# Kernel optimization log

Measured on AMD Instinct MI355X. Metric: run time of the kernel, lower is better.

## Reference

```python
import jax, jax.numpy as jnp
from jax import lax
import numpy as np

B, T, I, H = 4096, 200, 32, 6  # batch, seq_len, input_size, hidden


def _lstm_layer(x_seq, W_ih, W_hh, b_ih, b_hh):
    """Single unidirectional LSTM layer, PyTorch gate order (i,f,g,o).
    x_seq: [B,T,Din]. Returns (all_h [B,T,H], h_last [B,H])."""
    Bb = x_seq.shape[0]
    Hh = W_hh.shape[1]
    # Precompute input projections for all timesteps (hoisted out of the scan).
    x_proj = jnp.einsum('bti,gi->btg', x_seq, W_ih) + b_ih + b_hh  # [B,T,4H]

    def step(carry, xp_t):
        h, c = carry
        gates = xp_t + h @ W_hh.T  # [B,4H]
        i_g, f_g, g_g, o_g = jnp.split(gates, 4, axis=-1)
        i_g = jax.nn.sigmoid(i_g)
        f_g = jax.nn.sigmoid(f_g)
        g_g = jnp.tanh(g_g)
        o_g = jax.nn.sigmoid(o_g)
        c = f_g * c + i_g * g_g
        h = o_g * jnp.tanh(c)
        return (h, c), h

    init = (jnp.zeros((Bb, Hh), x_seq.dtype), jnp.zeros((Bb, Hh), x_seq.dtype))
    (h_last, _), hs = lax.scan(step, init, jnp.swapaxes(x_proj, 0, 1))  # time-major scan
    return jnp.swapaxes(hs, 0, 1), h_last


def setup_inputs() -> dict:
    key = jax.random.key(0)
    ks = jax.random.split(key, 11)
    s = 0.2  # ~ uniform(-1/sqrt(H)) scale for H=6
    inp = {
        'x': jax.random.normal(ks[0], (B, T, I), dtype=jnp.float32),
        'W_ih0': jax.random.normal(ks[1], (4 * H, I), dtype=jnp.float32) * s,
        'W_hh0': jax.random.normal(ks[2], (4 * H, H), dtype=jnp.float32) * s,
        'b_ih0': jax.random.normal(ks[3], (4 * H,), dtype=jnp.float32) * s,
        'b_hh0': jax.random.normal(ks[4], (4 * H,), dtype=jnp.float32) * s,
        'W_ih1': jax.random.normal(ks[5], (4 * H, H), dtype=jnp.float32) * s,
        'W_hh1': jax.random.normal(ks[6], (4 * H, H), dtype=jnp.float32) * s,
        'b_ih1': jax.random.normal(ks[7], (4 * H,), dtype=jnp.float32) * s,
        'b_hh1': jax.random.normal(ks[8], (4 * H,), dtype=jnp.float32) * s,
        'W_lin': jax.random.normal(ks[9], (1, H), dtype=jnp.float32) * s,
        'b_lin': jax.random.normal(ks[10], (1,), dtype=jnp.float32) * s,
    }
    return inp


def reference(x, W_ih0, W_hh0, b_ih0, b_hh0, W_ih1, W_hh1, b_ih1, b_hh1, W_lin, b_lin):
    # Layer 0 (eval mode: inter-layer dropout disabled)
    h1_seq, _ = _lstm_layer(x, W_ih0, W_hh0, b_ih0, b_hh0)
    # Layer 1
    _, h2_last = _lstm_layer(h1_seq, W_ih1, W_hh1, b_ih1, b_hh1)
    # Linear head on last layer's final hidden state: [B,1]
    return h2_last @ W_lin.T + b_lin
```

## Files before the change

kernel.cpp:

```cpp
#include <hip/hip_runtime.h>


#define TLEN  200
#define ISZ   32
#define HSZ   6
#define RPITCH 25
#define WPITCH 36
#define RING_DW (64 * RPITCH)
#define WOFF  RING_DW
#define BOFF  (WOFF + 24 * WPITCH)
#define LDS_DW (BOFF + 24)

__device__ __forceinline__ float fast_sig(float x) {
    return __builtin_amdgcn_rcpf(1.0f + __expf(-x));
}
__device__ __forceinline__ float rl(float v, int l) {
    return __int_as_float(__builtin_amdgcn_readlane(__float_as_int(v), l));
}
template <int CTRL>
__device__ __forceinline__ float qperm(float v) {
    return __int_as_float(__builtin_amdgcn_mov_dpp(__float_as_int(v), CTRL, 0xf, 0xf, true));
}
__device__ __forceinline__ float dot4(float4 w, float4 v) {
    return fmaf(w.x, v.x, fmaf(w.y, v.y, fmaf(w.z, v.z, w.w * v.w)));
}

__global__ __launch_bounds__(64) void lstm_one(
    const float* __restrict__ x,
    const float* __restrict__ Wih0, const float* __restrict__ Whh0,
    const float* __restrict__ bih0, const float* __restrict__ bhh0,
    const float* __restrict__ Wih1, const float* __restrict__ Whh1,
    const float* __restrict__ bih1, const float* __restrict__ bhh1,
    const float* __restrict__ Wlin, const float* __restrict__ blin,
    float* __restrict__ out)
{
    __shared__ float lds[LDS_DW];

    const int lane = threadIdx.x;
    const int b    = blockIdx.x;

    const int o = lane & 1;
    const int L = lane >> 1;

    const bool loHalf = (lane < 32);
    const int  p  = lane & 3;
    const int  jq = (lane & 31) >> 2;
    const int  j  = (jq < HSZ) ? jq : 0;
    const int  r  = 6 * p + j;

#define LDSW(ROW, KCQ) (*(const float4*)&lds[WOFF + (o * 12 + (ROW)) * WPITCH + ((KCQ) << 2)])

#pragma unroll
    for (int k = 0; k < 13; ++k) {
        const int idx = lane + (k << 6);
        if (idx < 768) {
            const int row = idx >> 5, kk = idx & 31;
            lds[WOFF + row * WPITCH + kk] = Wih0[idx];
        } else if (idx < 792) {
            lds[BOFF + idx - 768] = bih0[idx - 768] + bhh0[idx - 768];
        }
    }

    float WA[6], WB[6], base1 = 0.0f, sgc = 1.0f, tgc = 0.0f;
#pragma unroll
    for (int k = 0; k < 6; ++k) { WA[k] = 0.0f; WB[k] = 0.0f; }
    if (loHalf) {
#pragma unroll
        for (int k = 0; k < 6; ++k) WA[k] = Whh0[r * 6 + k];
    } else {
#pragma unroll
        for (int k = 0; k < 6; ++k) { WA[k] = Wih1[r * 6 + k]; WB[k] = Whh1[r * 6 + k]; }
        base1 = bih1[r] + bhh1[r];
    }
    if (p == 2) {
#pragma unroll
        for (int k = 0; k < 6; ++k) { WA[k] *= 2.0f; WB[k] *= 2.0f; }
        base1 *= 2.0f; sgc = 2.0f; tgc = -1.0f;
    }

    const float* xb = x + (size_t)b * TLEN * ISZ;

#pragma unroll
    for (int w01 = 0; w01 < 2; ++w01) {
        const int t = (w01 << 5) + L;
        const float4* xr4 = (const float4*)(xb + t * ISZ);
        float4 xw[8];
#pragma unroll
        for (int q = 0; q < 8; ++q) xw[q] = xr4[q];
        float a0c[12];
#pragma unroll
        for (int jj = 0; jj < 12; ++jj) a0c[jj] = 0.0f;
#pragma unroll
        for (int kc = 0; kc < 8; ++kc)
#pragma unroll
            for (int jj = 0; jj < 12; ++jj)
                a0c[jj] += dot4(LDSW(jj, kc), xw[kc]);
#pragma unroll
        for (int jj = 0; jj < 12; ++jj) {
            float v = a0c[jj] + lds[BOFF + o * 12 + jj];
            if (jj < 6) v = (o == 1) ? v * 2.0f : v;
            lds[t * RPITCH + o * 12 + jj] = v;
        }
    }

    float acc[12];
#pragma unroll
    for (int jj = 0; jj < 12; ++jj) acc[jj] = 0.0f;
    const float* pc = xb + (size_t)min(64 + L, TLEN - 1) * ISZ;
    const float* pn = xb + (size_t)min(96 + L, TLEN - 1) * ISZ;
    float4 f0, f1;
    f1 = *((const float4*)pc);
    float4 Wp0 = LDSW(0, 0), Wp1 = LDSW(1, 0), Wp2 = LDSW(2, 0);

    float c = 0.0f, h = 0.0f;
    float xp_cur = lds[r];

#define KC_HEAD(KC) do { \
    f0 = f1; \
    const float4* _srcp = ((KC) < 7) ? ((const float4*)pc + (KC) + 1) \
                                     : ((const float4*)pn); \
    f1 = *_srcp; \
} while (0)

#define SPREAD_STEP(RT, KC) do { \
    acc[3*(RT)+0] += dot4(Wp0, f0); \
    acc[3*(RT)+1] += dot4(Wp1, f0); \
    acc[3*(RT)+2] += dot4(Wp2, f0); \
    const int _rtn = ((RT) + 1) & 3; \
    const int _kcn = ((RT) == 3) ? (((KC) + 1) & 7) : (KC); \
    Wp0 = LDSW(3*_rtn + 0, _kcn); \
    Wp1 = LDSW(3*_rtn + 1, _kcn); \
    Wp2 = LDSW(3*_rtn + 2, _kcn); \
} while (0)

#define SCAN_STEP(ITV) do { \
    const float h10=rl(h,0),  h11=rl(h,4),  h12=rl(h,8); \
    const float h13=rl(h,12), h14=rl(h,16), h15=rl(h,20); \
    const float h20=rl(h,32), h21=rl(h,36), h22=rl(h,40); \
    const float h23=rl(h,44), h24=rl(h,48), h25=rl(h,52); \
    const float _xn = lds[(((ITV) + 1) & 63) * RPITCH + r]; \
    const float _g0 = loHalf ? xp_cur : base1; \
    const float _a0 = fmaf(WA[0],h10, fmaf(WA[2],h12, fmaf(WA[4],h14, _g0))); \
    const float _a1 = fmaf(WA[1],h11, fmaf(WA[3],h13, WA[5]*h15)); \
    const float _b0 = fmaf(WB[0],h20, fmaf(WB[2],h22, WB[4]*h24)); \
    const float _b1 = fmaf(WB[1],h21, fmaf(WB[3],h23, WB[5]*h25)); \
    const float _g  = (_a0 + _a1) + (_b0 + _b1); \
    const float _aG = fmaf(sgc, fast_sig(_g), tgc); \
    const float _iq = qperm<0x00>(_aG), _fq = qperm<0x55>(_aG); \
    const float _gq = qperm<0xAA>(_aG), _oq = qperm<0xFF>(_aG); \
    c = fmaf(_fq, c, _iq * _gq); \
    const float _th = fmaf(2.0f, fast_sig(2.0f * c), -1.0f); \
    h = _oq * _th; \
    xp_cur = _xn; \
    if ((ITV) == 200) { \
        float _s = blin[0]; \
        _s = fmaf(Wlin[0], rl(h, 32), _s); \
        _s = fmaf(Wlin[1], rl(h, 36), _s); \
        _s = fmaf(Wlin[2], rl(h, 40), _s); \
        _s = fmaf(Wlin[3], rl(h, 44), _s); \
        _s = fmaf(Wlin[4], rl(h, 48), _s); \
        _s = fmaf(Wlin[5], rl(h, 52), _s); \
        if (lane == 0) out[b] = _s; \
    } \
} while (0)

#define ENTRY(IT0) do { \
    const int _slot = ((IT0) + 32 + L) & 63; \
    _Pragma("unroll") \
    for (int _jj = 0; _jj < 12; ++_jj) { \
        float _v = acc[_jj] + lds[BOFF + o * 12 + _jj]; \
        if (_jj < 6) _v = (o == 1) ? _v * 2.0f : _v; \
        lds[_slot * RPITCH + o * 12 + _jj] = _v; \
        acc[_jj] = 0.0f; \
    } \
    pc = pn; \
    pn = xb + (size_t)min((IT0) + 96 + L, TLEN - 1) * ISZ; \
} while (0)

    KC_HEAD(0);
    SPREAD_STEP(0, 0);
    {
        const float g  = loHalf ? xp_cur : base1;
        const float aG = fmaf(sgc, fast_sig(g), tgc);
        const float iq = qperm<0x00>(aG), gq = qperm<0xAA>(aG), oq = qperm<0xFF>(aG);
        const float cn = iq * gq;
        const float th = fmaf(2.0f, fast_sig(2.0f * cn), -1.0f);
        c = loHalf ? cn : 0.0f;
        h = loHalf ? (oq * th) : 0.0f;
        xp_cur = lds[RPITCH + r];
    }

    SPREAD_STEP(1, 0); SCAN_STEP(1);
    SPREAD_STEP(2, 0); SCAN_STEP(2);
    SPREAD_STEP(3, 0); SCAN_STEP(3);
    for (int kc = 1; kc < 8; ++kc) {
        KC_HEAD(kc);
        const int itb = kc << 2;
        SPREAD_STEP(0, kc); SCAN_STEP(itb + 0);
        SPREAD_STEP(1, kc); SCAN_STEP(itb + 1);
        SPREAD_STEP(2, kc); SCAN_STEP(itb + 2);
        SPREAD_STEP(3, kc); SCAN_STEP(itb + 3);
    }

    for (int w = 1; w < 7; ++w) {
        const int it0 = w << 5;
        ENTRY(it0);
        for (int kc = 0; kc < 8; ++kc) {
            const int itb = it0 + (kc << 2);
            if (itb > 200) break;
            KC_HEAD(kc);
            SPREAD_STEP(0, kc); SCAN_STEP(itb + 0);
            SPREAD_STEP(1, kc); SCAN_STEP(itb + 1);
            SPREAD_STEP(2, kc); SCAN_STEP(itb + 2);
            SPREAD_STEP(3, kc); SCAN_STEP(itb + 3);
        }
    }

#undef LDSW
#undef KC_HEAD
#undef SPREAD_STEP
#undef SCAN_STEP
#undef ENTRY
}

extern "C" void kernel_launch(void* const* d_in, const int* in_sizes, int n_in,
                              void* d_out, int out_size, void* d_ws, size_t ws_size,
                              hipStream_t stream) {
    const float* x    = (const float*)d_in[0];
    const float* Wih0 = (const float*)d_in[1];
    const float* Whh0 = (const float*)d_in[2];
    const float* bih0 = (const float*)d_in[3];
    const float* bhh0 = (const float*)d_in[4];
    const float* Wih1 = (const float*)d_in[5];
    const float* Whh1 = (const float*)d_in[6];
    const float* bih1 = (const float*)d_in[7];
    const float* bhh1 = (const float*)d_in[8];
    const float* Wlin = (const float*)d_in[9];
    const float* blin = (const float*)d_in[10];
    float* out = (float*)d_out;

    lstm_one<<<4096, 64, 0, stream>>>(x, Wih0, Whh0, bih0, bhh0,
                                      Wih1, Whh1, bih1, bhh1,
                                      Wlin, blin, out);
}
```

Before: 249.8 us.

## Split input projection into a producer wave feeding the scan wave via LDS

Adds a second wavefront per block that computes the layer-0 input projections for 32-timestep windows into a double-buffered LDS ring. The original wave now runs only the recurrent scan, with raised scheduling priority, and the two waves sync with barriers at each window boundary. This takes the projection FMAs and global x loads off the serial scan's critical path. In exchange it doubles threads per block, which may reduce resident blocks, and adds barrier stalls each window.

```diff
diff --git a/kernel.cpp b/kernel.cpp
--- a/kernel.cpp
+++ b/kernel.cpp
@@ -25,7 +25,7 @@
     return fmaf(w.x, v.x, fmaf(w.y, v.y, fmaf(w.z, v.z, w.w * v.w)));
 }
 
-__global__ __launch_bounds__(64) void lstm_one(
+__global__ __launch_bounds__(128) void lstm_one(
     const float* __restrict__ x,
     const float* __restrict__ Wih0, const float* __restrict__ Whh0,
     const float* __restrict__ bih0, const float* __restrict__ bhh0,
@@ -36,11 +36,68 @@
 {
     __shared__ float lds[LDS_DW];
 
-    const int lane = threadIdx.x;
+    const int tid  = threadIdx.x;
+    const int lane = tid & 63;
     const int b    = blockIdx.x;
-
-    const int o = lane & 1;
-    const int L = lane >> 1;
+    const float* xb = x + (size_t)b * TLEN * ISZ;
+
+    if (tid >= 64) {
+        const int o = lane & 1;
+        const int L = lane >> 1;
+#define LDSW(ROW, KCQ) (*(const float4*)&lds[WOFF + (o * 12 + (ROW)) * WPITCH + ((KCQ) << 2)])
+
+#pragma unroll
+        for (int k = 0; k < 13; ++k) {
+            const int idx = lane + (k << 6);
+            if (idx < 768) {
+                const int row = idx >> 5, kk = idx & 31;
+                lds[WOFF + row * WPITCH + kk] = Wih0[idx];
+            } else if (idx < 792) {
+                lds[BOFF + idx - 768] = bih0[idx - 768] + bhh0[idx - 768];
+            }
+        }
+
+        float a0c[12];
+        auto PROJW = [&](int w) {
+            const int t = (w << 5) + L;
+            const float4* xr4 = (const float4*)(xb + (size_t)min(t, TLEN - 1) * ISZ);
+#pragma unroll
+            for (int jj = 0; jj < 12; ++jj) a0c[jj] = 0.0f;
+#pragma unroll
+            for (int hh = 0; hh < 2; ++hh) {
+                float4 xw[4];
+#pragma unroll
+                for (int q = 0; q < 4; ++q) xw[q] = xr4[(hh << 2) + q];
+#pragma unroll
+                for (int kc = 0; kc < 4; ++kc)
+#pragma unroll
+                    for (int jj = 0; jj < 12; ++jj)
+                        a0c[jj] += dot4(LDSW(jj, (hh << 2) + kc), xw[kc]);
+            }
+        };
+        auto WRITEW = [&](int w) {
+            const int slot = ((w << 5) + L) & 63;
+#pragma unroll
+            for (int jj = 0; jj < 12; ++jj) {
+                float v = a0c[jj] + lds[BOFF + o * 12 + jj];
+                if (jj < 6) v = (o == 1) ? v * 2.0f : v;
+                lds[slot * RPITCH + o * 12 + jj] = v;
+            }
+        };
+
+        PROJW(0); WRITEW(0);
+        PROJW(1); WRITEW(1);
+        __syncthreads();
+#pragma unroll 1
+        for (int w = 2; w < 7; ++w) {
+            PROJW(w);
+            __syncthreads();
+            WRITEW(w);
+            __syncthreads();
+        }
+#undef LDSW
+        return;
+    }
 
     const bool loHalf = (lane < 32);
     const int  p  = lane & 3;
@@ -48,19 +105,6 @@
     const int  j  = (jq < HSZ) ? jq : 0;
     const int  r  = 6 * p + j;
 
-#define LDSW(ROW, KCQ) (*(const float4*)&lds[WOFF + (o * 12 + (ROW)) * WPITCH + ((KCQ) << 2)])
-
-#pragma unroll
-    for (int k = 0; k < 13; ++k) {
-        const int idx = lane + (k << 6);
-        if (idx < 768) {
-            const int row = idx >> 5, kk = idx & 31;
-            lds[WOFF + row * WPITCH + kk] = Wih0[idx];
-        } else if (idx < 792) {
-            lds[BOFF + idx - 768] = bih0[idx - 768] + bhh0[idx - 768];
-        }
-    }
-
     float WA[6], WB[6], base1 = 0.0f, sgc = 1.0f, tgc = 0.0f;
 #pragma unroll
     for (int k = 0; k < 6; ++k) { WA[k] = 0.0f; WB[k] = 0.0f; }
@@ -78,72 +122,24 @@
         base1 *= 2.0f; sgc = 2.0f; tgc = -1.0f;
     }
 
-    const float* xb = x + (size_t)b * TLEN * ISZ;
-
-#pragma unroll
-    for (int w01 = 0; w01 < 2; ++w01) {
-        const int t = (w01 << 5) + L;
-        const float4* xr4 = (const float4*)(xb + t * ISZ);
-        float4 xw[8];
-#pragma unroll
-        for (int q = 0; q < 8; ++q) xw[q] = xr4[q];
-        float a0c[12];
-#pragma unroll
-        for (int jj = 0; jj < 12; ++jj) a0c[jj] = 0.0f;
-#pragma unroll
-        for (int kc = 0; kc < 8; ++kc)
-#pragma unroll
-            for (int jj = 0; jj < 12; ++jj)
-                a0c[jj] += dot4(LDSW(jj, kc), xw[kc]);
-#pragma unroll
-        for (int jj = 0; jj < 12; ++jj) {
-            float v = a0c[jj] + lds[BOFF + o * 12 + jj];
-            if (jj < 6) v = (o == 1) ? v * 2.0f : v;
-            lds[t * RPITCH + o * 12 + jj] = v;
-        }
-    }
-
-    float acc[12];
-#pragma unroll
-    for (int jj = 0; jj < 12; ++jj) acc[jj] = 0.0f;
-    const float* pc = xb + (size_t)min(64 + L, TLEN - 1) * ISZ;
-    const float* pn = xb + (size_t)min(96 + L, TLEN - 1) * ISZ;
-    float4 f0, f1;
-    f1 = *((const float4*)pc);
-    float4 Wp0 = LDSW(0, 0), Wp1 = LDSW(1, 0), Wp2 = LDSW(2, 0);
-
+    __syncthreads();
+    __builtin_amdgcn_s_setprio(1);
+
+    int xoff = r;
     float c = 0.0f, h = 0.0f;
-    float xp_cur = lds[r];
-
-#define KC_HEAD(KC) do { \
-    f0 = f1; \
-    const float4* _srcp = ((KC) < 7) ? ((const float4*)pc + (KC) + 1) \
-                                     : ((const float4*)pn); \
-    f1 = *_srcp; \
-} while (0)
-
-#define SPREAD_STEP(RT, KC) do { \
-    acc[3*(RT)+0] += dot4(Wp0, f0); \
-    acc[3*(RT)+1] += dot4(Wp1, f0); \
-    acc[3*(RT)+2] += dot4(Wp2, f0); \
-    const int _rtn = ((RT) + 1) & 3; \
-    const int _kcn = ((RT) == 3) ? (((KC) + 1) & 7) : (KC); \
-    Wp0 = LDSW(3*_rtn + 0, _kcn); \
-    Wp1 = LDSW(3*_rtn + 1, _kcn); \
-    Wp2 = LDSW(3*_rtn + 2, _kcn); \
-} while (0)
-
-#define SCAN_STEP(ITV) do { \
-    const float h10=rl(h,0),  h11=rl(h,4),  h12=rl(h,8); \
-    const float h13=rl(h,12), h14=rl(h,16), h15=rl(h,20); \
-    const float h20=rl(h,32), h21=rl(h,36), h22=rl(h,40); \
-    const float h23=rl(h,44), h24=rl(h,48), h25=rl(h,52); \
-    const float _xn = lds[(((ITV) + 1) & 63) * RPITCH + r]; \
+    float xp_cur = lds[xoff];
+
+#define SCAN_STEP(XN) do { \
+    const float h10 = rl(h, 0),  h11 = rl(h, 4),  h12 = rl(h, 8); \
+    const float h13 = rl(h, 12), h14 = rl(h, 16), h15 = rl(h, 20); \
+    const float h20 = rl(h, 32), h21 = rl(h, 36), h22 = rl(h, 40); \
+    const float h23 = rl(h, 44), h24 = rl(h, 48), h25 = rl(h, 52); \
+    const float _xn = (XN); \
     const float _g0 = loHalf ? xp_cur : base1; \
-    const float _a0 = fmaf(WA[0],h10, fmaf(WA[2],h12, fmaf(WA[4],h14, _g0))); \
-    const float _a1 = fmaf(WA[1],h11, fmaf(WA[3],h13, WA[5]*h15)); \
-    const float _b0 = fmaf(WB[0],h20, fmaf(WB[2],h22, WB[4]*h24)); \
-    const float _b1 = fmaf(WB[1],h21, fmaf(WB[3],h23, WB[5]*h25)); \
+    const float _a0 = fmaf(WA[0], h10, fmaf(WA[2], h12, fmaf(WA[4], h14, _g0))); \
+    const float _a1 = fmaf(WA[1], h11, fmaf(WA[3], h13, WA[5] * h15)); \
+    const float _b0 = fmaf(WB[0], h20, fmaf(WB[2], h22, WB[4] * h24)); \
+    const float _b1 = fmaf(WB[1], h21, fmaf(WB[3], h23, WB[5] * h25)); \
     const float _g  = (_a0 + _a1) + (_b0 + _b1); \
     const float _aG = fmaf(sgc, fast_sig(_g), tgc); \
     const float _iq = qperm<0x00>(_aG), _fq = qperm<0x55>(_aG); \
@@ -152,33 +148,8 @@
     const float _th = fmaf(2.0f, fast_sig(2.0f * c), -1.0f); \
     h = _oq * _th; \
     xp_cur = _xn; \
-    if ((ITV) == 200) { \
-        float _s = blin[0]; \
-        _s = fmaf(Wlin[0], rl(h, 32), _s); \
-        _s = fmaf(Wlin[1], rl(h, 36), _s); \
-        _s = fmaf(Wlin[2], rl(h, 40), _s); \
-        _s = fmaf(Wlin[3], rl(h, 44), _s); \
-        _s = fmaf(Wlin[4], rl(h, 48), _s); \
-        _s = fmaf(Wlin[5], rl(h, 52), _s); \
-        if (lane == 0) out[b] = _s; \
-    } \
 } while (0)
 
-#define ENTRY(IT0) do { \
-    const int _slot = ((IT0) + 32 + L) & 63; \
-    _Pragma("unroll") \
-    for (int _jj = 0; _jj < 12; ++_jj) { \
-        float _v = acc[_jj] + lds[BOFF + o * 12 + _jj]; \
-        if (_jj < 6) _v = (o == 1) ? _v * 2.0f : _v; \
-        lds[_slot * RPITCH + o * 12 + _jj] = _v; \
-        acc[_jj] = 0.0f; \
-    } \
-    pc = pn; \
-    pn = xb + (size_t)min((IT0) + 96 + L, TLEN - 1) * ISZ; \
-} while (0)
-
-    KC_HEAD(0);
-    SPREAD_STEP(0, 0);
     {
         const float g  = loHalf ? xp_cur : base1;
         const float aG = fmaf(sgc, fast_sig(g), tgc);
@@ -187,40 +158,33 @@
         const float th = fmaf(2.0f, fast_sig(2.0f * cn), -1.0f);
         c = loHalf ? cn : 0.0f;
         h = loHalf ? (oq * th) : 0.0f;
-        xp_cur = lds[RPITCH + r];
-    }
-
-    SPREAD_STEP(1, 0); SCAN_STEP(1);
-    SPREAD_STEP(2, 0); SCAN_STEP(2);
-    SPREAD_STEP(3, 0); SCAN_STEP(3);
-    for (int kc = 1; kc < 8; ++kc) {
-        KC_HEAD(kc);
-        const int itb = kc << 2;
-        SPREAD_STEP(0, kc); SCAN_STEP(itb + 0);
-        SPREAD_STEP(1, kc); SCAN_STEP(itb + 1);
-        SPREAD_STEP(2, kc); SCAN_STEP(itb + 2);
-        SPREAD_STEP(3, kc); SCAN_STEP(itb + 3);
-    }
-
-    for (int w = 1; w < 7; ++w) {
-        const int it0 = w << 5;
-        ENTRY(it0);
-        for (int kc = 0; kc < 8; ++kc) {
-            const int itb = it0 + (kc << 2);
-            if (itb > 200) break;
-            KC_HEAD(kc);
-            SPREAD_STEP(0, kc); SCAN_STEP(itb + 0);
-            SPREAD_STEP(1, kc); SCAN_STEP(itb + 1);
-            SPREAD_STEP(2, kc); SCAN_STEP(itb + 2);
-            SPREAD_STEP(3, kc); SCAN_STEP(itb + 3);
-        }
-    }
-
-#undef LDSW
-#undef KC_HEAD
-#undef SPREAD_STEP
+        xp_cur = lds[xoff + RPITCH];
+    }
+
+#pragma unroll 1
+    for (int w = 0; w < 6; ++w) {
+        if (w > 0) SCAN_STEP(lds[xoff + RPITCH]);
+#pragma unroll
+        for (int k = 1; k <= 30; ++k) SCAN_STEP(lds[xoff + (k + 1) * RPITCH]);
+        xoff ^= 800;
+        SCAN_STEP(lds[xoff]);
+        if (w < 5) { __syncthreads(); __syncthreads(); }
+    }
+
+#pragma unroll
+    for (int k = 0; k < 8; ++k) SCAN_STEP(lds[xoff + (k + 1) * RPITCH]);
+    SCAN_STEP(lds[xoff + 9 * RPITCH]);
+    {
+        float s = blin[0];
+        s = fmaf(Wlin[0], rl(h, 32), s);
+        s = fmaf(Wlin[1], rl(h, 36), s);
+        s = fmaf(Wlin[2], rl(h, 40), s);
+        s = fmaf(Wlin[3], rl(h, 44), s);
+        s = fmaf(Wlin[4], rl(h, 48), s);
+        s = fmaf(Wlin[5], rl(h, 52), s);
+        if (lane == 0) out[b] = s;
+    }
 #undef SCAN_STEP
-#undef ENTRY
 }
 
 extern "C" void kernel_launch(void* const* d_in, const int* in_sizes, int n_in,
@@ -239,7 +203,7 @@
     const float* blin = (const float*)d_in[10];
     float* out = (float*)d_out;
 
-    lstm_one<<<4096, 64, 0, stream>>>(x, Wih0, Whh0, bih0, bhh0,
-                                      Wih1, Whh1, bih1, bhh1,
-                                      Wlin, blin, out);
-}
+    lstm_one<<<4096, 128, 0, stream>>>(x, Wih0, Whh0, bih0, bhh0,
+                                       Wih1, Whh1, bih1, bhh1,
+                                       Wlin, blin, out);
+}
```

After: 355.0 us. +42.1%, slower.

## Split LSTM into global-memory input projection phase then recurrent scan

Applied to the files above, without the earlier changes.

Adds a kernel variant that first computes all layer-0 input projections for a sequence and writes them to a workspace buffer in global memory. It then runs the two-layer recurrence as a separate phase that prefetches projections from that buffer, four steps ahead. This replaces the interleaved LDS ring that mixed projection math into the scan, shrinking LDS use and simplifying the critical recurrent loop. The cost is about 78 MB of extra global write and read traffic, plus a full wait before the scan starts. The old fused kernel remains as a fallback when the workspace is too small.

```diff
diff --git a/kernel.cpp b/kernel.cpp
--- a/kernel.cpp
+++ b/kernel.cpp
@@ -4,12 +4,17 @@
 #define TLEN  200
 #define ISZ   32
 #define HSZ   6
+#define WPITCH 36
+
+#define PWOFF 0
+#define PBOFF (24 * WPITCH)
+#define PLDS_DW (PBOFF + 24)
+
 #define RPITCH 25
-#define WPITCH 36
 #define RING_DW (64 * RPITCH)
-#define WOFF  RING_DW
-#define BOFF  (WOFF + 24 * WPITCH)
-#define LDS_DW (BOFF + 24)
+#define FWOFF  RING_DW
+#define FBOFF  (FWOFF + 24 * WPITCH)
+#define FLDS_DW (FBOFF + 24)
 
 __device__ __forceinline__ float fast_sig(float x) {
     return __builtin_amdgcn_rcpf(1.0f + __expf(-x));
@@ -25,7 +30,170 @@
     return fmaf(w.x, v.x, fmaf(w.y, v.y, fmaf(w.z, v.z, w.w * v.w)));
 }
 
-__global__ __launch_bounds__(64) void lstm_one(
+__global__ __launch_bounds__(64) void lstm_split(
+    const float* __restrict__ x,
+    const float* __restrict__ Wih0, const float* __restrict__ Whh0,
+    const float* __restrict__ bih0, const float* __restrict__ bhh0,
+    const float* __restrict__ Wih1, const float* __restrict__ Whh1,
+    const float* __restrict__ bih1, const float* __restrict__ bhh1,
+    const float* __restrict__ Wlin, const float* __restrict__ blin,
+    float* __restrict__ out, float* __restrict__ xp)
+{
+    __shared__ float lds[PLDS_DW];
+
+    const int lane = threadIdx.x;
+    const int b    = blockIdx.x;
+    const float* xb  = x  + (size_t)b * TLEN * ISZ;
+    float*       xpb = xp + (size_t)b * TLEN * 24;
+
+    {
+        const int o = lane & 1;
+        const int L = lane >> 1;
+#define LDSW(ROW, KCQ) (*(const float4*)&lds[PWOFF + (o * 12 + (ROW)) * WPITCH + ((KCQ) << 2)])
+
+#pragma unroll
+        for (int k = 0; k < 13; ++k) {
+            const int idx = lane + (k << 6);
+            if (idx < 768) {
+                const int row = idx >> 5, kk = idx & 31;
+                lds[PWOFF + row * WPITCH + kk] = Wih0[idx];
+            } else if (idx < 792) {
+                lds[PBOFF + idx - 768] = bih0[idx - 768] + bhh0[idx - 768];
+            }
+        }
+
+#pragma unroll 1
+        for (int k7 = 0; k7 < 7; ++k7) {
+            const int t = (k7 << 5) + L;
+            if (t < TLEN) {
+                const float4* xr4 = (const float4*)(xb + (size_t)t * ISZ);
+                float a0c[12];
+#pragma unroll
+                for (int jj = 0; jj < 12; ++jj) a0c[jj] = 0.0f;
+#pragma unroll
+                for (int hh = 0; hh < 2; ++hh) {
+                    float4 xw[4];
+#pragma unroll
+                    for (int q = 0; q < 4; ++q) xw[q] = xr4[(hh << 2) + q];
+#pragma unroll
+                    for (int jh = 0; jh < 2; ++jh)
+#pragma unroll
+                        for (int kc = 0; kc < 4; ++kc)
+#pragma unroll
+                            for (int jj = jh * 6; jj < jh * 6 + 6; ++jj)
+                                a0c[jj] += dot4(LDSW(jj, (hh << 2) + kc), xw[kc]);
+                }
+                float vv[12];
+#pragma unroll
+                for (int jj = 0; jj < 12; ++jj) {
+                    float v = a0c[jj] + lds[PBOFF + o * 12 + jj];
+                    if (jj < 6) v = (o == 1) ? v * 2.0f : v;
+                    vv[jj] = v;
+                }
+                float4* dst = (float4*)(xpb + t * 24 + o * 12);
+                dst[0] = make_float4(vv[0], vv[1], vv[2],  vv[3]);
+                dst[1] = make_float4(vv[4], vv[5], vv[6],  vv[7]);
+                dst[2] = make_float4(vv[8], vv[9], vv[10], vv[11]);
+            }
+        }
+#undef LDSW
+    }
+
+    asm volatile("s_waitcnt vmcnt(0)" ::: "memory");
+
+    const bool loHalf = (lane < 32);
+    const int  p  = lane & 3;
+    const int  jq = (lane & 31) >> 2;
+    const int  j  = (jq < HSZ) ? jq : 0;
+    const int  r  = 6 * p + j;
+
+    float WA[6], WB[6], base1 = 0.0f, sgc = 1.0f, tgc = 0.0f;
+#pragma unroll
+    for (int k = 0; k < 6; ++k) { WA[k] = 0.0f; WB[k] = 0.0f; }
+    if (loHalf) {
+#pragma unroll
+        for (int k = 0; k < 6; ++k) WA[k] = Whh0[r * 6 + k];
+    } else {
+#pragma unroll
+        for (int k = 0; k < 6; ++k) { WA[k] = Wih1[r * 6 + k]; WB[k] = Whh1[r * 6 + k]; }
+        base1 = bih1[r] + bhh1[r];
+    }
+    if (p == 2) {
+#pragma unroll
+        for (int k = 0; k < 6; ++k) { WA[k] *= 2.0f; WB[k] *= 2.0f; }
+        base1 *= 2.0f; sgc = 2.0f; tgc = -1.0f;
+    }
+
+    const float* xr = xpb + r;
+    float xp0 = xr[0];
+    float q0 = xr[24], q1 = xr[48], q2 = xr[72], q3 = xr[96];
+
+    float c = 0.0f, h = 0.0f;
+
+#define SSTEP(XPV) do { \
+    const float h10 = rl(h, 0),  h11 = rl(h, 4),  h12 = rl(h, 8); \
+    const float h13 = rl(h, 12), h14 = rl(h, 16), h15 = rl(h, 20); \
+    const float h20 = rl(h, 32), h21 = rl(h, 36), h22 = rl(h, 40); \
+    const float h23 = rl(h, 44), h24 = rl(h, 48), h25 = rl(h, 52); \
+    const float _g0 = loHalf ? (XPV) : base1; \
+    const float _a0 = fmaf(WA[0], h10, fmaf(WA[2], h12, fmaf(WA[4], h14, _g0))); \
+    const float _a1 = fmaf(WA[1], h11, fmaf(WA[3], h13, WA[5] * h15)); \
+    const float _b0 = fmaf(WB[0], h20, fmaf(WB[2], h22, WB[4] * h24)); \
+    const float _b1 = fmaf(WB[1], h21, fmaf(WB[3], h23, WB[5] * h25)); \
+    const float _g  = (_a0 + _a1) + (_b0 + _b1); \
+    const float _aG = fmaf(sgc, fast_sig(_g), tgc); \
+    const float _iq = qperm<0x00>(_aG), _fq = qperm<0x55>(_aG); \
+    const float _gq = qperm<0xAA>(_aG), _oq = qperm<0xFF>(_aG); \
+    c = fmaf(_fq, c, _iq * _gq); \
+    const float _th = fmaf(2.0f, fast_sig(2.0f * c), -1.0f); \
+    h = _oq * _th; \
+} while (0)
+
+    {
+        const float g  = loHalf ? xp0 : base1;
+        const float aG = fmaf(sgc, fast_sig(g), tgc);
+        const float iq = qperm<0x00>(aG), gq = qperm<0xAA>(aG), oq = qperm<0xFF>(aG);
+        const float cn = iq * gq;
+        const float th = fmaf(2.0f, fast_sig(2.0f * cn), -1.0f);
+        c = loHalf ? cn : 0.0f;
+        h = loHalf ? (oq * th) : 0.0f;
+    }
+
+    const float* P = xr + 24;
+#pragma unroll 1
+    for (int bod = 0; bod < 24; ++bod) {
+        SSTEP(q0); q0 = P[4 * 24];
+        SSTEP(q1); q1 = P[5 * 24];
+        SSTEP(q2); q2 = P[6 * 24];
+        SSTEP(q3); q3 = P[7 * 24];
+        SSTEP(q0); q0 = P[8 * 24];
+        SSTEP(q1); q1 = P[9 * 24];
+        SSTEP(q2); q2 = P[10 * 24];
+        SSTEP(q3); q3 = P[11 * 24];
+        P += 8 * 24;
+    }
+    SSTEP(q0); q0 = P[4 * 24];
+    SSTEP(q1); q1 = P[5 * 24];
+    SSTEP(q2); q2 = P[6 * 24];
+    SSTEP(q3);
+    SSTEP(q0);
+    SSTEP(q1);
+    SSTEP(q2);
+    SSTEP(q3);
+    {
+        float s = blin[0];
+        s = fmaf(Wlin[0], rl(h, 32), s);
+        s = fmaf(Wlin[1], rl(h, 36), s);
+        s = fmaf(Wlin[2], rl(h, 40), s);
+        s = fmaf(Wlin[3], rl(h, 44), s);
+        s = fmaf(Wlin[4], rl(h, 48), s);
+        s = fmaf(Wlin[5], rl(h, 52), s);
+        if (lane == 0) out[b] = s;
+    }
+#undef SSTEP
+}
+
+__global__ __launch_bounds__(64) void lstm_fb(
     const float* __restrict__ x,
     const float* __restrict__ Wih0, const float* __restrict__ Whh0,
     const float* __restrict__ bih0, const float* __restrict__ bhh0,
@@ -34,7 +202,7 @@
     const float* __restrict__ Wlin, const float* __restrict__ blin,
     float* __restrict__ out)
 {
-    __shared__ float lds[LDS_DW];
+    __shared__ float lds[FLDS_DW];
 
     const int lane = threadIdx.x;
     const int b    = blockIdx.x;
@@ -48,16 +216,16 @@
     const int  j  = (jq < HSZ) ? jq : 0;
     const int  r  = 6 * p + j;
 
-#define LDSW(ROW, KCQ) (*(const float4*)&lds[WOFF + (o * 12 + (ROW)) * WPITCH + ((KCQ) << 2)])
+#define LDSW(ROW, KCQ) (*(const float4*)&lds[FWOFF + (o * 12 + (ROW)) * WPITCH + ((KCQ) << 2)])
 
 #pragma unroll
     for (int k = 0; k < 13; ++k) {
         const int idx = lane + (k << 6);
         if (idx < 768) {
             const int row = idx >> 5, kk = idx & 31;
-            lds[WOFF + row * WPITCH + kk] = Wih0[idx];
+            lds[FWOFF + row * WPITCH + kk] = Wih0[idx];
         } else if (idx < 792) {
-            lds[BOFF + idx - 768] = bih0[idx - 768] + bhh0[idx - 768];
+            lds[FBOFF + idx - 768] = bih0[idx - 768] + bhh0[idx - 768];
         }
     }
 
@@ -97,7 +265,7 @@
                 a0c[jj] += dot4(LDSW(jj, kc), xw[kc]);
 #pragma unroll
         for (int jj = 0; jj < 12; ++jj) {
-            float v = a0c[jj] + lds[BOFF + o * 12 + jj];
+            float v = a0c[jj] + lds[FBOFF + o * 12 + jj];
             if (jj < 6) v = (o == 1) ? v * 2.0f : v;
             lds[t * RPITCH + o * 12 + jj] = v;
         }
@@ -168,7 +336,7 @@
     const int _slot = ((IT0) + 32 + L) & 63; \
     _Pragma("unroll") \
     for (int _jj = 0; _jj < 12; ++_jj) { \
-        float _v = acc[_jj] + lds[BOFF + o * 12 + _jj]; \
+        float _v = acc[_jj] + lds[FBOFF + o * 12 + _jj]; \
         if (_jj < 6) _v = (o == 1) ? _v * 2.0f : _v; \
         lds[_slot * RPITCH + o * 12 + _jj] = _v; \
         acc[_jj] = 0.0f; \
@@ -239,7 +407,14 @@
     const float* blin = (const float*)d_in[10];
     float* out = (float*)d_out;
 
-    lstm_one<<<4096, 64, 0, stream>>>(x, Wih0, Whh0, bih0, bhh0,
-                                      Wih1, Whh1, bih1, bhh1,
-                                      Wlin, blin, out);
-}
+    const size_t XP_BYTES = (size_t)4096 * TLEN * 24 * sizeof(float);
+    if (d_ws != nullptr && ws_size >= XP_BYTES) {
+        lstm_split<<<4096, 64, 0, stream>>>(x, Wih0, Whh0, bih0, bhh0,
+                                            Wih1, Whh1, bih1, bhh1,
+                                            Wlin, blin, out, (float*)d_ws);
+    } else {
+        lstm_fb<<<4096, 64, 0, stream>>>(x, Wih0, Whh0, bih0, bhh0,
+                                         Wih1, Whh1, bih1, bhh1,
+                                         Wlin, blin, out);
+    }
+}
```

New measurement: 268.6 us. +7.5%, slower.

## Split LSTM into projection kernel and packed 4-batch-per-wave scan kernel

Applied to the files above, without the earlier changes.

Replaces the single fused kernel with two kernels when a workspace is available. The first computes the layer-0 input projections for all timesteps into global memory. The second runs the recurrence with four batch elements per 64-lane wave, each lane owning one hidden unit and computing all four gates, with ds_swizzle broadcasts instead of readlane. This packs lanes more densely and removes the in-loop projection work from the serial chain. In exchange it writes and reads about 79 MB of projections through global memory. It keeps the old kernel as a fallback.

```diff
diff --git a/kernel.cpp b/kernel.cpp
--- a/kernel.cpp
+++ b/kernel.cpp
@@ -4,15 +4,26 @@
 #define TLEN  200
 #define ISZ   32
 #define HSZ   6
+#define WPITCH 36
+
+#define PWOFF 0
+#define PBOFF (24 * WPITCH)
+#define PLDS_DW (PBOFF + 24)
+
 #define RPITCH 25
-#define WPITCH 36
 #define RING_DW (64 * RPITCH)
-#define WOFF  RING_DW
-#define BOFF  (WOFF + 24 * WPITCH)
-#define LDS_DW (BOFF + 24)
+#define FWOFF  RING_DW
+#define FBOFF  (FWOFF + 24 * WPITCH)
+#define FLDS_DW (FBOFF + 24)
+
+#define XP4_COUNT ((size_t)4096 * TLEN * 6)
+#define WS_REQ    ((XP4_COUNT + 6) * 16)
 
 __device__ __forceinline__ float fast_sig(float x) {
     return __builtin_amdgcn_rcpf(1.0f + __expf(-x));
+}
+__device__ __forceinline__ float tanh_s(float x) {
+    return fmaf(2.0f, fast_sig(x + x), -1.0f);
 }
 __device__ __forceinline__ float rl(float v, int l) {
     return __int_as_float(__builtin_amdgcn_readlane(__float_as_int(v), l));
@@ -21,11 +32,170 @@
 __device__ __forceinline__ float qperm(float v) {
     return __int_as_float(__builtin_amdgcn_mov_dpp(__float_as_int(v), CTRL, 0xf, 0xf, true));
 }
+template <int OFF>
+__device__ __forceinline__ float swz(float v) {
+    return __int_as_float(__builtin_amdgcn_ds_swizzle(__float_as_int(v), OFF));
+}
 __device__ __forceinline__ float dot4(float4 w, float4 v) {
     return fmaf(w.x, v.x, fmaf(w.y, v.y, fmaf(w.z, v.z, w.w * v.w)));
 }
 
-__global__ __launch_bounds__(64) void lstm_one(
+__global__ __launch_bounds__(64) void proj_k(
+    const float* __restrict__ x,    const float* __restrict__ Wih0,
+    const float* __restrict__ bih0, const float* __restrict__ bhh0,
+    const float* __restrict__ bih1, const float* __restrict__ bhh1,
+    float4* __restrict__ xp4)
+{
+    __shared__ float lds[PLDS_DW];
+    const int lane = threadIdx.x;
+    const int b    = blockIdx.x;
+    const int o = lane & 1;
+    const int L = lane >> 1;
+    const float* xb = x + (size_t)b * TLEN * ISZ;
+
+#pragma unroll
+    for (int k = 0; k < 13; ++k) {
+        const int idx = lane + (k << 6);
+        if (idx < 768) {
+            const int row = idx >> 5, kk = idx & 31;
+            const int slot = ((row % 6) / 3) * 12 + (row / 6) * 3 + (row % 3);
+            lds[PWOFF + slot * WPITCH + kk] = Wih0[idx];
+        } else if (idx < 792) {
+            const int r = idx - 768;
+            const int slot = ((r % 6) / 3) * 12 + (r / 6) * 3 + (r % 3);
+            lds[PBOFF + slot] = bih0[r] + bhh0[r];
+        }
+    }
+    if (blockIdx.x == 0 && lane < 24) {
+        const int u = lane % 6, g = lane / 6;
+        ((float*)(xp4 + XP4_COUNT))[u * 4 + g] = bih1[g * 6 + u] + bhh1[g * 6 + u];
+    }
+
+#define PLDSW(ROW, KCQ) (*(const float4*)&lds[PWOFF + (o * 12 + (ROW)) * WPITCH + ((KCQ) << 2)])
+#pragma unroll 1
+    for (int w = 0; w < 7; ++w) {
+        const int t = (w << 5) + L;
+        if (t < TLEN) {
+            const float4* xr4 = (const float4*)(xb + (size_t)t * ISZ);
+            float a0c[12];
+#pragma unroll
+            for (int jj = 0; jj < 12; ++jj) a0c[jj] = 0.0f;
+#pragma unroll
+            for (int hh = 0; hh < 2; ++hh) {
+                float4 xw[4];
+#pragma unroll
+                for (int q = 0; q < 4; ++q) xw[q] = xr4[(hh << 2) + q];
+#pragma unroll
+                for (int jh = 0; jh < 2; ++jh)
+#pragma unroll
+                    for (int kc = 0; kc < 4; ++kc)
+#pragma unroll
+                        for (int jj = jh * 6; jj < jh * 6 + 6; ++jj)
+                            a0c[jj] += dot4(PLDSW(jj, (hh << 2) + kc), xw[kc]);
+            }
+            float vv[12];
+#pragma unroll
+            for (int jj = 0; jj < 12; ++jj) vv[jj] = a0c[jj] + lds[PBOFF + o * 12 + jj];
+            float4* dst = xp4 + ((size_t)b * TLEN + t) * 6 + 3 * o;
+#pragma unroll
+            for (int v = 0; v < 3; ++v)
+                dst[v] = make_float4(vv[v], vv[3 + v], vv[6 + v], vv[9 + v]);
+        }
+    }
+#undef PLDSW
+}
+
+__global__ __launch_bounds__(64) void lstm_scan(
+    const float* __restrict__ Whh0, const float* __restrict__ Wih1,
+    const float* __restrict__ Whh1, const float* __restrict__ Wlin,
+    const float* __restrict__ blin, const float4* __restrict__ xp4,
+    float* __restrict__ out)
+{
+    const int lane = threadIdx.x;
+    const int role = lane & 15;
+    const int grp  = lane >> 4;
+    const int b    = blockIdx.x * 4 + grp;
+
+    float WA[4][6], WB[4][6];
+#pragma unroll
+    for (int g = 0; g < 4; ++g)
+#pragma unroll
+        for (int k = 0; k < 6; ++k) { WA[g][k] = 0.0f; WB[g][k] = 0.0f; }
+    if (role < 6) {
+#pragma unroll
+        for (int g = 0; g < 4; ++g)
+#pragma unroll
+            for (int k = 0; k < 6; ++k) WA[g][k] = Whh0[(g * 6 + role) * 6 + k];
+    } else if (role < 12) {
+        const int u = role - 6;
+#pragma unroll
+        for (int g = 0; g < 4; ++g)
+#pragma unroll
+            for (int k = 0; k < 6; ++k) {
+                WA[g][k] = Wih1[(g * 6 + u) * 6 + k];
+                WB[g][k] = Whh1[(g * 6 + u) * 6 + k];
+            }
+    }
+    const float4* P;
+    int ST;
+    if (role < 6) { P = xp4 + (size_t)b * TLEN * 6 + role; ST = 6; }
+    else          { P = xp4 + XP4_COUNT + (role < 12 ? role - 6 : 0); ST = 0; }
+
+    float4 q0 = P[0], q1 = P[ST], q2 = P[2 * ST], q3 = P[3 * ST];
+    P += 4 * ST;
+
+    float c = 0.0f, h = 0.0f;
+
+#define STEP(XQ) do { \
+    const float hA0 = swz<0x010>(h), hA1 = swz<0x030>(h), hA2 = swz<0x050>(h); \
+    const float hA3 = swz<0x070>(h), hA4 = swz<0x090>(h), hA5 = swz<0x0B0>(h); \
+    const float hB0 = swz<0x0D0>(h), hB1 = swz<0x0F0>(h), hB2 = swz<0x110>(h); \
+    const float hB3 = swz<0x130>(h), hB4 = swz<0x150>(h), hB5 = swz<0x170>(h); \
+    float a0 = (XQ).x, a1 = (XQ).y, a2 = (XQ).z, a3 = (XQ).w; \
+    ARG(a0, 0); ARG(a1, 1); ARG(a2, 2); ARG(a3, 3); \
+    const float ig = fast_sig(a0), fg = fast_sig(a1); \
+    const float gg = tanh_s(a2),   og = fast_sig(a3); \
+    c = fmaf(fg, c, ig * gg); \
+    h = og * tanh_s(c); \
+} while (0)
+
+#define ARG(A, G) do { \
+    const float s0 = fmaf(WA[G][0], hA0, fmaf(WA[G][1], hA1, fmaf(WA[G][2], hA2, A))); \
+    const float s1 = fmaf(WA[G][3], hA3, fmaf(WA[G][4], hA4, WA[G][5] * hA5)); \
+    const float s2 = fmaf(WB[G][0], hB0, fmaf(WB[G][1], hB1, WB[G][2] * hB2)); \
+    const float s3 = fmaf(WB[G][3], hB3, fmaf(WB[G][4], hB4, WB[G][5] * hB5)); \
+    A = (s0 + s1) + (s2 + s3); \
+} while (0)
+
+#define STEPR(QV) do { const float4 _xq = QV; QV = *P; P += ST; STEP(_xq); } while (0)
+
+    STEPR(q0);
+    h = (role < 6) ? h : 0.0f;
+    c = (role < 6) ? c : 0.0f;
+
+#pragma unroll 1
+    for (int m = 0; m < 48; ++m) {
+        STEPR(q1); STEPR(q2); STEPR(q3); STEPR(q0);
+    }
+    STEPR(q1); STEPR(q2); STEPR(q3);
+    STEP(q0); STEP(q1); STEP(q2); STEP(q3);
+    STEP(q0);
+
+    {
+        const float f0 = swz<0x0D0>(h), f1 = swz<0x0F0>(h), f2 = swz<0x110>(h);
+        const float f3 = swz<0x130>(h), f4 = swz<0x150>(h), f5 = swz<0x170>(h);
+        float s = blin[0];
+        s = fmaf(Wlin[0], f0, s); s = fmaf(Wlin[1], f1, s);
+        s = fmaf(Wlin[2], f2, s); s = fmaf(Wlin[3], f3, s);
+        s = fmaf(Wlin[4], f4, s); s = fmaf(Wlin[5], f5, s);
+        if (role == 0) out[b] = s;
+    }
+#undef STEP
+#undef ARG
+#undef STEPR
+}
+
+__global__ __launch_bounds__(64) void lstm_fb(
     const float* __restrict__ x,
     const float* __restrict__ Wih0, const float* __restrict__ Whh0,
     const float* __restrict__ bih0, const float* __restrict__ bhh0,
@@ -34,7 +204,7 @@
     const float* __restrict__ Wlin, const float* __restrict__ blin,
     float* __restrict__ out)
 {
-    __shared__ float lds[LDS_DW];
+    __shared__ float lds[FLDS_DW];
 
     const int lane = threadIdx.x;
     const int b    = blockIdx.x;
@@ -48,16 +218,16 @@
     const int  j  = (jq < HSZ) ? jq : 0;
     const int  r  = 6 * p + j;
 
-#define LDSW(ROW, KCQ) (*(const float4*)&lds[WOFF + (o * 12 + (ROW)) * WPITCH + ((KCQ) << 2)])
+#define LDSW(ROW, KCQ) (*(const float4*)&lds[FWOFF + (o * 12 + (ROW)) * WPITCH + ((KCQ) << 2)])
 
 #pragma unroll
     for (int k = 0; k < 13; ++k) {
         const int idx = lane + (k << 6);
         if (idx < 768) {
             const int row = idx >> 5, kk = idx & 31;
-            lds[WOFF + row * WPITCH + kk] = Wih0[idx];
+            lds[FWOFF + row * WPITCH + kk] = Wih0[idx];
         } else if (idx < 792) {
-            lds[BOFF + idx - 768] = bih0[idx - 768] + bhh0[idx - 768];
+            lds[FBOFF + idx - 768] = bih0[idx - 768] + bhh0[idx - 768];
         }
     }
 
@@ -97,7 +267,7 @@
                 a0c[jj] += dot4(LDSW(jj, kc), xw[kc]);
 #pragma unroll
         for (int jj = 0; jj < 12; ++jj) {
-            float v = a0c[jj] + lds[BOFF + o * 12 + jj];
+            float v = a0c[jj] + lds[FBOFF + o * 12 + jj];
             if (jj < 6) v = (o == 1) ? v * 2.0f : v;
             lds[t * RPITCH + o * 12 + jj] = v;
         }
@@ -168,7 +338,7 @@
     const int _slot = ((IT0) + 32 + L) & 63; \
     _Pragma("unroll") \
     for (int _jj = 0; _jj < 12; ++_jj) { \
-        float _v = acc[_jj] + lds[BOFF + o * 12 + _jj]; \
+        float _v = acc[_jj] + lds[FBOFF + o * 12 + _jj]; \
         if (_jj < 6) _v = (o == 1) ? _v * 2.0f : _v; \
         lds[_slot * RPITCH + o * 12 + _jj] = _v; \
         acc[_jj] = 0.0f; \
@@ -239,7 +409,14 @@
     const float* blin = (const float*)d_in[10];
     float* out = (float*)d_out;
 
-    lstm_one<<<4096, 64, 0, stream>>>(x, Wih0, Whh0, bih0, bhh0,
-                                      Wih1, Whh1, bih1, bhh1,
-                                      Wlin, blin, out);
-}
+    if (d_ws != nullptr && ws_size >= WS_REQ) {
+        float4* xp4 = (float4*)d_ws;
+        proj_k<<<4096, 64, 0, stream>>>(x, Wih0, bih0, bhh0, bih1, bhh1, xp4);
+        lstm_scan<<<1024, 64, 0, stream>>>(Whh0, Wih1, Whh1, Wlin, blin,
+                                           (const float4*)xp4, out);
+    } else {
+        lstm_fb<<<4096, 64, 0, stream>>>(x, Wih0, Whh0, bih0, bhh0,
+                                         Wih1, Whh1, bih1, bhh1,
+                                         Wlin, blin, out);
+    }
+}
```

After: 253.2 us. About the same (+1.4%).
